# Optimization experiments

Hardware: AMD Instinct MI355X
Metric: run time of the kernel (lower is better)

## Reference

```python
import jax, jax.numpy as jnp
import numpy as np

N = 50000


def gcn_conv(x, edge_index, W, b):
    # x: [N, F_in], edge_index: [2, E] (row=source j, col=target i)
    n = x.shape[0]
    loops = jnp.arange(n, dtype=edge_index.dtype)
    row = jnp.concatenate([edge_index[0], loops])
    col = jnp.concatenate([edge_index[1], loops])
    # linear transform first (PyG GCNConv)
    xw = x @ W  # [N, F_out]
    # symmetric normalization deg^{-1/2}[row] * deg^{-1/2}[col]
    deg = jax.ops.segment_sum(jnp.ones_like(col, dtype=xw.dtype), col, num_segments=n)
    dis = jnp.where(deg > 0, jax.lax.rsqrt(jnp.maximum(deg, 1e-12)), 0.0)
    norm = dis[row] * dis[col]  # [E+N]
    # gather-scale-scatter: sum_j norm_ij * (W x_j)
    msgs = xw[row] * norm[:, None]
    out = jax.ops.segment_sum(msgs, col, num_segments=n)
    return out + b


def setup_inputs() -> dict:
    key = jax.random.key(0)
    k1, k2, k3, k4, k5 = jax.random.split(key, 5)
    in_dim, hidden_dim, out_dim = 128, 128, 64
    x = jax.random.normal(k1, (N, in_dim), dtype=jnp.float32)
    edge_index = jax.random.randint(k2, (2, 800000), 0, N, dtype=jnp.int64)
    s1 = 1.0 / np.sqrt(in_dim)
    s2 = 1.0 / np.sqrt(hidden_dim)
    W1 = jax.random.uniform(k3, (in_dim, hidden_dim), jnp.float32, -s1, s1)
    b1 = jnp.zeros((hidden_dim,), jnp.float32)
    W2 = jax.random.uniform(k4, (hidden_dim, out_dim), jnp.float32, -s2, s2)
    b2 = jnp.zeros((out_dim,), jnp.float32)
    return {"x": x, "edge_index": edge_index, "W1": W1, "b1": b1, "W2": W2, "b2": b2}


def reference(x, edge_index, W1, b1, W2, b2):
    h = gcn_conv(x, edge_index, W1, b1)
    h = jax.nn.relu(h)
    # dropout(p=0.5, training=False) -> identity (inference reference)
    out = gcn_conv(h, edge_index, W2, b2)
    return out
```

## Files before the change

kernel.cpp:

```cpp
#include <hip/hip_runtime.h>
#include <hip/hip_fp16.h>


typedef _Float16 half8 __attribute__((ext_vector_type(8)));
typedef float floatx4 __attribute__((ext_vector_type(4)));

__global__ void k_count(const int* __restrict__ col, int* __restrict__ deg,
                        int* __restrict__ rank, int E) {
    int e = blockIdx.x * blockDim.x + threadIdx.x;
    if (e < E) rank[e] = atomicAdd(&deg[col[e]], 1);
}

__global__ __launch_bounds__(1024) void k_scan_local(const int* __restrict__ deg,
                                                     int* __restrict__ rowptr,
                                                     int* __restrict__ bsum,
                                                     float* __restrict__ dis, int n) {
    __shared__ int s[1024];
    int b = blockIdx.x, tid = threadIdx.x;
    int i = b * 1024 + tid;
    int v = (i < n) ? deg[i] : 0;
    if (i < n) dis[i] = rsqrtf((float)v + 1.0f);
    s[tid] = v;
    __syncthreads();
    for (int off = 1; off < 1024; off <<= 1) {
        int t = (tid >= off) ? s[tid - off] : 0;
        __syncthreads();
        s[tid] += t;
        __syncthreads();
    }
    if (i < n) rowptr[i + 1] = s[tid];
    if (tid == 1023) bsum[b] = s[1023];
    if (b == 0 && tid == 0) rowptr[0] = 0;
}

__global__ __launch_bounds__(256) void k_scan_fix(int* __restrict__ rowptr,
                                                  const int* __restrict__ bsum, int n) {
    __shared__ int red[256];
    int b = blockIdx.x, tid = threadIdx.x;
    int partial = 0;
    for (int j = tid; j < b; j += 256) partial += bsum[j];
    red[tid] = partial;
    __syncthreads();
    for (int off = 128; off > 0; off >>= 1) {
        if (tid < off) red[tid] += red[tid + off];
        __syncthreads();
    }
    int offv = red[0];
    if (offv == 0) return;
#pragma unroll
    for (int r = 0; r < 4; ++r) {
        int i = b * 1024 + r * 256 + tid;
        if (i < n) rowptr[i + 1] += offv;
    }
}

__global__ void k_fill(const int* __restrict__ row, const int* __restrict__ col,
                       const int* __restrict__ rowptr, const int* __restrict__ rank,
                       int* __restrict__ csr, int E) {
    int e = blockIdx.x * blockDim.x + threadIdx.x;
    if (e < E) csr[rowptr[col[e]] + rank[e]] = row[e];
}

template <int N, typename AT>
__global__ __launch_bounds__(256) void k_gemm_mfma(const AT* __restrict__ X,
                                                   const float* __restrict__ W,
                                                   const float* __restrict__ scale,
                                                   __half* __restrict__ Y, int M) {
    __shared__ __align__(16) __half2 wt[N * 64];
    int tid = threadIdx.x;
    for (int i = tid; i < N * 64; i += 256) {
        int n = i & (N - 1);
        int k2 = i / N;
        float w0 = W[(size_t)(2 * k2) * N + n];
        float w1 = W[(size_t)(2 * k2 + 1) * N + n];
        wt[n * 64 + ((k2 >> 2) ^ (n & 15)) * 4 + (k2 & 3)] = __floats2half2_rn(w0, w1);
    }
    __syncthreads();

    int wid = tid >> 6, lane = tid & 63;
    int col = lane & 15, quad = lane >> 4;
    int m_a = blockIdx.x * 64 + wid * 16 + col;
    bool a_ok = m_a < M;
    constexpr int NT = N / 16;
    floatx4 acc[NT] = {};
#pragma unroll
    for (int ks = 0; ks < 4; ++ks) {
        int k = ks * 32 + quad * 8;
        half8 af;
        if constexpr (sizeof(AT) == 4) {
            floatx4 a0 = {0.f, 0.f, 0.f, 0.f}, a1 = {0.f, 0.f, 0.f, 0.f};
            if (a_ok) {
                a0 = *(const floatx4*)&X[(size_t)m_a * 128 + k];
                a1 = *(const floatx4*)&X[(size_t)m_a * 128 + k + 4];
            }
            af = half8{(_Float16)a0[0], (_Float16)a0[1], (_Float16)a0[2], (_Float16)a0[3],
                       (_Float16)a1[0], (_Float16)a1[1], (_Float16)a1[2], (_Float16)a1[3]};
        } else {
            half8 t = {};
            if (a_ok) t = *(const half8*)(const void*)&X[(size_t)m_a * 128 + k];
            af = t;
        }
        int kblk = ks * 4 + quad;
#pragma unroll
        for (int nt = 0; nt < NT; ++nt) {
            int n = nt * 16 + col;
            half8 bf = *(const half8*)(const void*)&wt[n * 64 + (kblk ^ (n & 15)) * 4];
            acc[nt] = __builtin_amdgcn_mfma_f32_16x16x32_f16(af, bf, acc[nt], 0, 0, 0);
        }
    }
    int mbase = blockIdx.x * 64 + wid * 16 + quad * 4;
    float s[4];
#pragma unroll
    for (int r = 0; r < 4; ++r) s[r] = (mbase + r < M) ? scale[mbase + r] : 0.f;
#pragma unroll
    for (int nt = 0; nt < NT; ++nt) {
#pragma unroll
        for (int r = 0; r < 4; ++r) {
            if (mbase + r < M)
                Y[(size_t)(mbase + r) * N + nt * 16 + col] = __float2half(acc[nt][r] * s[r]);
        }
    }
}

__global__ __launch_bounds__(256) void k_agg128(const __half* __restrict__ xw,
                                                const float* __restrict__ dis,
                                                const int* __restrict__ rowptr,
                                                const int* __restrict__ csr,
                                                const float* __restrict__ bias,
                                                __half* __restrict__ out, int n) {
    int tid = threadIdx.x;
    int lane = tid & 63;
    int q = lane >> 4, li = lane & 15;
    int node = blockIdx.x * 16 + ((tid >> 6) << 2) + q;
    bool ok = node < n;
    float di = 0.f;
    int beg = 0, end = 0;
    if (ok) {
        di = dis[node];
        beg = rowptr[node];
        end = rowptr[node + 1];
    }
    int deg = end - beg;
    int m1 = max(deg, __shfl(deg, lane ^ 16));
    int mx = max(m1, __shfl(m1, lane ^ 32));
    const half8* rows = (const half8*)xw;
    float acc[8] = {};
    if (ok) {
        half8 sf = rows[(size_t)node * 16 + li];
#pragma unroll
        for (int f = 0; f < 8; ++f) acc[f] = (float)sf[f];
    }
    int i = 0;
    for (; i + 8 <= mx; i += 8) {
        int s[8];
        half8 v[8];
#pragma unroll
        for (int j = 0; j < 8; ++j) {
            int e = beg + i + j;
            s[j] = (e < end) ? csr[e] : 0;
        }
#pragma unroll
        for (int j = 0; j < 8; ++j) v[j] = rows[(size_t)s[j] * 16 + li];
#pragma unroll
        for (int j = 0; j < 8; ++j) {
            if (beg + i + j < end) {
#pragma unroll
                for (int f = 0; f < 8; ++f) acc[f] += (float)v[j][f];
            }
        }
    }
    for (; i < mx; ++i) {
        int e = beg + i;
        int s = (e < end) ? csr[e] : 0;
        half8 v = rows[(size_t)s * 16 + li];
        if (e < end) {
#pragma unroll
            for (int f = 0; f < 8; ++f) acc[f] += (float)v[f];
        }
    }
    if (ok) {
        floatx4 b0 = *(const floatx4*)&bias[li * 8];
        floatx4 b1 = *(const floatx4*)&bias[li * 8 + 4];
        half8 o;
#pragma unroll
        for (int f = 0; f < 4; ++f) o[f] = (_Float16)fmaxf(acc[f] * di + b0[f], 0.f);
#pragma unroll
        for (int f = 0; f < 4; ++f) o[4 + f] = (_Float16)fmaxf(acc[4 + f] * di + b1[f], 0.f);
        ((half8*)out)[(size_t)node * 16 + li] = o;
    }
}

__global__ __launch_bounds__(256) void k_agg64(const __half* __restrict__ xw,
                                               const float* __restrict__ dis,
                                               const int* __restrict__ rowptr,
                                               const int* __restrict__ csr,
                                               const float* __restrict__ bias,
                                               float* __restrict__ out, int n) {
    int tid = threadIdx.x;
    int lane = tid & 63;
    int o8 = lane >> 3, li = lane & 7;
    int node = blockIdx.x * 32 + ((tid >> 6) << 3) + o8;
    bool ok = node < n;
    float di = 0.f;
    int beg = 0, end = 0;
    if (ok) {
        di = dis[node];
        beg = rowptr[node];
        end = rowptr[node + 1];
    }
    int deg = end - beg;
    int m1 = max(deg, __shfl(deg, lane ^ 8));
    int m2 = max(m1, __shfl(m1, lane ^ 16));
    int mx = max(m2, __shfl(m2, lane ^ 32));
    const half8* rows = (const half8*)xw;
    float acc[8] = {};
    if (ok) {
        half8 sf = rows[(size_t)node * 8 + li];
#pragma unroll
        for (int f = 0; f < 8; ++f) acc[f] = (float)sf[f];
    }
    int i = 0;
    for (; i + 8 <= mx; i += 8) {
        int s[8];
        half8 v[8];
#pragma unroll
        for (int j = 0; j < 8; ++j) {
            int e = beg + i + j;
            s[j] = (e < end) ? csr[e] : 0;
        }
#pragma unroll
        for (int j = 0; j < 8; ++j) v[j] = rows[(size_t)s[j] * 8 + li];
#pragma unroll
        for (int j = 0; j < 8; ++j) {
            if (beg + i + j < end) {
#pragma unroll
                for (int f = 0; f < 8; ++f) acc[f] += (float)v[j][f];
            }
        }
    }
    for (; i < mx; ++i) {
        int e = beg + i;
        int s = (e < end) ? csr[e] : 0;
        half8 v = rows[(size_t)s * 8 + li];
        if (e < end) {
#pragma unroll
            for (int f = 0; f < 8; ++f) acc[f] += (float)v[f];
        }
    }
    if (ok) {
        floatx4 b0 = *(const floatx4*)&bias[li * 8];
        floatx4 b1 = *(const floatx4*)&bias[li * 8 + 4];
        floatx4 o0, o1;
#pragma unroll
        for (int f = 0; f < 4; ++f) o0[f] = acc[f] * di + b0[f];
#pragma unroll
        for (int f = 0; f < 4; ++f) o1[f] = acc[4 + f] * di + b1[f];
        *(floatx4*)&out[(size_t)node * 64 + li * 8] = o0;
        *(floatx4*)&out[(size_t)node * 64 + li * 8 + 4] = o1;
    }
}

extern "C" void kernel_launch(void* const* d_in, const int* in_sizes, int n_in,
                              void* d_out, int out_size, void* d_ws, size_t ws_size,
                              hipStream_t stream) {
    const float* x  = (const float*)d_in[0];
    const int*   ei = (const int*)d_in[1];
    const float* W1 = (const float*)d_in[2];
    const float* b1 = (const float*)d_in[3];
    const float* W2 = (const float*)d_in[4];
    const float* b2 = (const float*)d_in[5];
    float* out = (float*)d_out;

    const int n = in_sizes[0] / 128;
    const int E = in_sizes[1] / 2;
    const int* row = ei;
    const int* col = ei + E;
    const int NB = (n + 1023) / 1024;

    char* ws = (char*)d_ws;
    size_t off = 0;
    auto alloc = [&](size_t bytes) -> void* {
        void* p = ws + off;
        off += (bytes + 255) & ~(size_t)255;
        return p;
    };
    int*    deg    = (int*)alloc((size_t)n * 4);
    int*    rowptr = (int*)alloc((size_t)(n + 1) * 4);
    int*    bsum   = (int*)alloc((size_t)NB * 4);
    int*    rank   = (int*)alloc((size_t)E * 4);
    int*    csr    = (int*)alloc((size_t)E * 4);
    float*  dis    = (float*)alloc((size_t)n * 4);
    __half* xw1    = (__half*)alloc((size_t)n * 128 * 2);
    __half* h      = (__half*)alloc((size_t)n * 128 * 2);
    __half* xw2    = (__half*)alloc((size_t)n * 64 * 2);
    (void)ws_size;

    hipMemsetAsync(deg, 0, (size_t)n * 4, stream);
    k_count<<<(E + 255) / 256, 256, 0, stream>>>(col, deg, rank, E);
    k_scan_local<<<NB, 1024, 0, stream>>>(deg, rowptr, bsum, dis, n);
    k_scan_fix<<<NB, 256, 0, stream>>>(rowptr, bsum, n);
    k_fill<<<(E + 255) / 256, 256, 0, stream>>>(row, col, rowptr, rank, csr, E);

    int gb = (n + 63) / 64;
    k_gemm_mfma<128, float><<<gb, 256, 0, stream>>>(x, W1, dis, xw1, n);
    k_agg128<<<(n + 15) / 16, 256, 0, stream>>>(xw1, dis, rowptr, csr, b1, h, n);

    k_gemm_mfma<64, __half><<<gb, 256, 0, stream>>>(h, W2, dis, xw2, n);
    k_agg64<<<(n + 31) / 32, 256, 0, stream>>>(xw2, dis, rowptr, csr, b2, out, n);
}
```

Baseline: 215.9 us.

## Fuse edge counting with first GEMM and store per-edge source norms in CSR

The degree-count atomics and the first MFMA GEMM now run as one launch, with blocks split by index, so the GEMM no longer depends on the degree scan. The GEMM drops its dis[row] scaling. Instead, the CSR fill stores each source's dis value next to its index as an int2, and the aggregation kernels apply that weight per edge; the bounds predicate is gone because padded entries carry a zero weight. This aims to overlap GEMM1 with the atomic counting pass and remove one kernel launch, at the cost of doubling CSR size and adding a multiply per feature per edge.

Result: slower. 226.5 us (+4.9%).

```diff
diff --git a/kernel.cpp b/kernel.cpp
--- a/kernel.cpp
+++ b/kernel.cpp
@@ -5,10 +5,80 @@
 typedef _Float16 half8 __attribute__((ext_vector_type(8)));
 typedef float floatx4 __attribute__((ext_vector_type(4)));
 
-__global__ void k_count(const int* __restrict__ col, int* __restrict__ deg,
-                        int* __restrict__ rank, int E) {
-    int e = blockIdx.x * blockDim.x + threadIdx.x;
-    if (e < E) rank[e] = atomicAdd(&deg[col[e]], 1);
+template <int N, typename AT>
+__device__ __forceinline__ void gemm_tile(const AT* __restrict__ X,
+                                          const float* __restrict__ W,
+                                          __half* __restrict__ Y, int M,
+                                          int m0, __half2* wt, int tid) {
+    for (int i = tid; i < N * 64; i += 256) {
+        int nn = i & (N - 1);
+        int k2 = i / N;
+        float w0 = W[(size_t)(2 * k2) * N + nn];
+        float w1 = W[(size_t)(2 * k2 + 1) * N + nn];
+        wt[nn * 64 + ((k2 >> 2) ^ (nn & 15)) * 4 + (k2 & 3)] = __floats2half2_rn(w0, w1);
+    }
+    __syncthreads();
+    int wid = tid >> 6, lane = tid & 63;
+    int col = lane & 15, quad = lane >> 4;
+    int m_a = m0 + wid * 16 + col;
+    bool a_ok = m_a < M;
+    constexpr int NT = N / 16;
+    floatx4 acc[NT] = {};
+#pragma unroll
+    for (int ks = 0; ks < 4; ++ks) {
+        int k = ks * 32 + quad * 8;
+        half8 af;
+        if constexpr (sizeof(AT) == 4) {
+            floatx4 a0 = {0.f, 0.f, 0.f, 0.f}, a1 = {0.f, 0.f, 0.f, 0.f};
+            if (a_ok) {
+                a0 = *(const floatx4*)&X[(size_t)m_a * 128 + k];
+                a1 = *(const floatx4*)&X[(size_t)m_a * 128 + k + 4];
+            }
+            af = half8{(_Float16)a0[0], (_Float16)a0[1], (_Float16)a0[2], (_Float16)a0[3],
+                       (_Float16)a1[0], (_Float16)a1[1], (_Float16)a1[2], (_Float16)a1[3]};
+        } else {
+            half8 t = {};
+            if (a_ok) t = *(const half8*)(const void*)&X[(size_t)m_a * 128 + k];
+            af = t;
+        }
+        int kblk = ks * 4 + quad;
+#pragma unroll
+        for (int nt = 0; nt < NT; ++nt) {
+            int nn = nt * 16 + col;
+            half8 bf = *(const half8*)(const void*)&wt[nn * 64 + (kblk ^ (nn & 15)) * 4];
+            acc[nt] = __builtin_amdgcn_mfma_f32_16x16x32_f16(af, bf, acc[nt], 0, 0, 0);
+        }
+    }
+    int mbase = m0 + wid * 16 + quad * 4;
+#pragma unroll
+    for (int nt = 0; nt < NT; ++nt) {
+#pragma unroll
+        for (int r = 0; r < 4; ++r) {
+            if (mbase + r < M)
+                Y[(size_t)(mbase + r) * N + nt * 16 + col] = __float2half(acc[nt][r]);
+        }
+    }
+}
+
+__global__ __launch_bounds__(256) void k_count_gemm1(
+    const int* __restrict__ col, int* __restrict__ deg, int* __restrict__ rank, int E,
+    const float* __restrict__ X, const float* __restrict__ W1,
+    __half* __restrict__ Y, int M, int CB) {
+    __shared__ __align__(16) __half2 wt[128 * 64];
+    int b = blockIdx.x, tid = threadIdx.x;
+    if (b < CB) {
+        int e = b * 256 + tid;
+        if (e < E) rank[e] = atomicAdd(&deg[col[e]], 1);
+        return;
+    }
+    gemm_tile<128, float>(X, W1, Y, M, (b - CB) * 64, wt, tid);
+}
+
+__global__ __launch_bounds__(256) void k_gemm2(const __half* __restrict__ X,
+                                               const float* __restrict__ W,
+                                               __half* __restrict__ Y, int M) {
+    __shared__ __align__(16) __half2 wt[64 * 64];
+    gemm_tile<64, __half>(X, W, Y, M, blockIdx.x * 64, wt, threadIdx.x);
 }
 
 __global__ __launch_bounds__(1024) void k_scan_local(const int* __restrict__ deg,
@@ -56,76 +126,18 @@
 
 __global__ void k_fill(const int* __restrict__ row, const int* __restrict__ col,
                        const int* __restrict__ rowptr, const int* __restrict__ rank,
-                       int* __restrict__ csr, int E) {
+                       const float* __restrict__ dis, int2* __restrict__ csrw, int E) {
     int e = blockIdx.x * blockDim.x + threadIdx.x;
-    if (e < E) csr[rowptr[col[e]] + rank[e]] = row[e];
-}
-
-template <int N, typename AT>
-__global__ __launch_bounds__(256) void k_gemm_mfma(const AT* __restrict__ X,
-                                                   const float* __restrict__ W,
-                                                   const float* __restrict__ scale,
-                                                   __half* __restrict__ Y, int M) {
-    __shared__ __align__(16) __half2 wt[N * 64];
-    int tid = threadIdx.x;
-    for (int i = tid; i < N * 64; i += 256) {
-        int n = i & (N - 1);
-        int k2 = i / N;
-        float w0 = W[(size_t)(2 * k2) * N + n];
-        float w1 = W[(size_t)(2 * k2 + 1) * N + n];
-        wt[n * 64 + ((k2 >> 2) ^ (n & 15)) * 4 + (k2 & 3)] = __floats2half2_rn(w0, w1);
-    }
-    __syncthreads();
-
-    int wid = tid >> 6, lane = tid & 63;
-    int col = lane & 15, quad = lane >> 4;
-    int m_a = blockIdx.x * 64 + wid * 16 + col;
-    bool a_ok = m_a < M;
-    constexpr int NT = N / 16;
-    floatx4 acc[NT] = {};
-#pragma unroll
-    for (int ks = 0; ks < 4; ++ks) {
-        int k = ks * 32 + quad * 8;
-        half8 af;
-        if constexpr (sizeof(AT) == 4) {
-            floatx4 a0 = {0.f, 0.f, 0.f, 0.f}, a1 = {0.f, 0.f, 0.f, 0.f};
-            if (a_ok) {
-                a0 = *(const floatx4*)&X[(size_t)m_a * 128 + k];
-                a1 = *(const floatx4*)&X[(size_t)m_a * 128 + k + 4];
-            }
-            af = half8{(_Float16)a0[0], (_Float16)a0[1], (_Float16)a0[2], (_Float16)a0[3],
-                       (_Float16)a1[0], (_Float16)a1[1], (_Float16)a1[2], (_Float16)a1[3]};
-        } else {
-            half8 t = {};
-            if (a_ok) t = *(const half8*)(const void*)&X[(size_t)m_a * 128 + k];
-            af = t;
-        }
-        int kblk = ks * 4 + quad;
-#pragma unroll
-        for (int nt = 0; nt < NT; ++nt) {
-            int n = nt * 16 + col;
-            half8 bf = *(const half8*)(const void*)&wt[n * 64 + (kblk ^ (n & 15)) * 4];
-            acc[nt] = __builtin_amdgcn_mfma_f32_16x16x32_f16(af, bf, acc[nt], 0, 0, 0);
-        }
-    }
-    int mbase = blockIdx.x * 64 + wid * 16 + quad * 4;
-    float s[4];
-#pragma unroll
-    for (int r = 0; r < 4; ++r) s[r] = (mbase + r < M) ? scale[mbase + r] : 0.f;
-#pragma unroll
-    for (int nt = 0; nt < NT; ++nt) {
-#pragma unroll
-        for (int r = 0; r < 4; ++r) {
-            if (mbase + r < M)
-                Y[(size_t)(mbase + r) * N + nt * 16 + col] = __float2half(acc[nt][r] * s[r]);
-        }
+    if (e < E) {
+        int r = row[e];
+        csrw[rowptr[col[e]] + rank[e]] = make_int2(r, __float_as_int(dis[r]));
     }
 }
 
 __global__ __launch_bounds__(256) void k_agg128(const __half* __restrict__ xw,
                                                 const float* __restrict__ dis,
                                                 const int* __restrict__ rowptr,
-                                                const int* __restrict__ csr,
+                                                const int2* __restrict__ csrw,
                                                 const float* __restrict__ bias,
                                                 __half* __restrict__ out, int n) {
     int tid = threadIdx.x;
@@ -140,43 +152,43 @@
         beg = rowptr[node];
         end = rowptr[node + 1];
     }
-    int deg = end - beg;
-    int m1 = max(deg, __shfl(deg, lane ^ 16));
+    int dg = end - beg;
+    int m1 = max(dg, __shfl(dg, lane ^ 16));
     int mx = max(m1, __shfl(m1, lane ^ 32));
     const half8* rows = (const half8*)xw;
     float acc[8] = {};
     if (ok) {
         half8 sf = rows[(size_t)node * 16 + li];
 #pragma unroll
-        for (int f = 0; f < 8; ++f) acc[f] = (float)sf[f];
+        for (int f = 0; f < 8; ++f) acc[f] = di * (float)sf[f];
     }
     int i = 0;
     for (; i + 8 <= mx; i += 8) {
         int s[8];
+        float w[8];
         half8 v[8];
 #pragma unroll
         for (int j = 0; j < 8; ++j) {
             int e = beg + i + j;
-            s[j] = (e < end) ? csr[e] : 0;
+            int2 cw = (e < end) ? csrw[e] : make_int2(0, 0);
+            s[j] = cw.x;
+            w[j] = __int_as_float(cw.y);
         }
 #pragma unroll
         for (int j = 0; j < 8; ++j) v[j] = rows[(size_t)s[j] * 16 + li];
 #pragma unroll
         for (int j = 0; j < 8; ++j) {
-            if (beg + i + j < end) {
-#pragma unroll
-                for (int f = 0; f < 8; ++f) acc[f] += (float)v[j][f];
-            }
+#pragma unroll
+            for (int f = 0; f < 8; ++f) acc[f] += w[j] * (float)v[j][f];
         }
     }
     for (; i < mx; ++i) {
         int e = beg + i;
-        int s = (e < end) ? csr[e] : 0;
-        half8 v = rows[(size_t)s * 16 + li];
-        if (e < end) {
-#pragma unroll
-            for (int f = 0; f < 8; ++f) acc[f] += (float)v[f];
-        }
+        int2 cw = (e < end) ? csrw[e] : make_int2(0, 0);
+        half8 v = rows[(size_t)cw.x * 16 + li];
+        float w = __int_as_float(cw.y);
+#pragma unroll
+        for (int f = 0; f < 8; ++f) acc[f] += w * (float)v[f];
     }
     if (ok) {
         floatx4 b0 = *(const floatx4*)&bias[li * 8];
@@ -193,7 +205,7 @@
 __global__ __launch_bounds__(256) void k_agg64(const __half* __restrict__ xw,
                                                const float* __restrict__ dis,
                                                const int* __restrict__ rowptr,
-                                               const int* __restrict__ csr,
+                                               const int2* __restrict__ csrw,
                                                const float* __restrict__ bias,
                                                float* __restrict__ out, int n) {
     int tid = threadIdx.x;
@@ -208,8 +220,8 @@
         beg = rowptr[node];
         end = rowptr[node + 1];
     }
-    int deg = end - beg;
-    int m1 = max(deg, __shfl(deg, lane ^ 8));
+    int dg = end - beg;
+    int m1 = max(dg, __shfl(dg, lane ^ 8));
     int m2 = max(m1, __shfl(m1, lane ^ 16));
     int mx = max(m2, __shfl(m2, lane ^ 32));
     const half8* rows = (const half8*)xw;
@@ -217,35 +229,35 @@
     if (ok) {
         half8 sf = rows[(size_t)node * 8 + li];
 #pragma unroll
-        for (int f = 0; f < 8; ++f) acc[f] = (float)sf[f];
+        for (int f = 0; f < 8; ++f) acc[f] = di * (float)sf[f];
     }
     int i = 0;
     for (; i + 8 <= mx; i += 8) {
         int s[8];
+        float w[8];
         half8 v[8];
 #pragma unroll
         for (int j = 0; j < 8; ++j) {
             int e = beg + i + j;
-            s[j] = (e < end) ? csr[e] : 0;
+            int2 cw = (e < end) ? csrw[e] : make_int2(0, 0);
+            s[j] = cw.x;
+            w[j] = __int_as_float(cw.y);
         }
 #pragma unroll
         for (int j = 0; j < 8; ++j) v[j] = rows[(size_t)s[j] * 8 + li];
 #pragma unroll
         for (int j = 0; j < 8; ++j) {
-            if (beg + i + j < end) {
-#pragma unroll
-                for (int f = 0; f < 8; ++f) acc[f] += (float)v[j][f];
-            }
+#pragma unroll
+            for (int f = 0; f < 8; ++f) acc[f] += w[j] * (float)v[j][f];
         }
     }
     for (; i < mx; ++i) {
         int e = beg + i;
-        int s = (e < end) ? csr[e] : 0;
-        half8 v = rows[(size_t)s * 8 + li];
-        if (e < end) {
-#pragma unroll
-            for (int f = 0; f < 8; ++f) acc[f] += (float)v[f];
-        }
+        int2 cw = (e < end) ? csrw[e] : make_int2(0, 0);
+        half8 v = rows[(size_t)cw.x * 8 + li];
+        float w = __int_as_float(cw.y);
+#pragma unroll
+        for (int f = 0; f < 8; ++f) acc[f] += w * (float)v[f];
     }
     if (ok) {
         floatx4 b0 = *(const floatx4*)&bias[li * 8];
@@ -276,6 +288,8 @@
     const int* row = ei;
     const int* col = ei + E;
     const int NB = (n + 1023) / 1024;
+    const int CB = (E + 255) / 256;
+    const int GB = (n + 63) / 64;
 
     char* ws = (char*)d_ws;
     size_t off = 0;
@@ -288,7 +302,7 @@
     int*    rowptr = (int*)alloc((size_t)(n + 1) * 4);
     int*    bsum   = (int*)alloc((size_t)NB * 4);
     int*    rank   = (int*)alloc((size_t)E * 4);
-    int*    csr    = (int*)alloc((size_t)E * 4);
+    int2*   csrw   = (int2*)alloc((size_t)E * 8);
     float*  dis    = (float*)alloc((size_t)n * 4);
     __half* xw1    = (__half*)alloc((size_t)n * 128 * 2);
     __half* h      = (__half*)alloc((size_t)n * 128 * 2);
@@ -296,15 +310,12 @@
     (void)ws_size;
 
     hipMemsetAsync(deg, 0, (size_t)n * 4, stream);
-    k_count<<<(E + 255) / 256, 256, 0, stream>>>(col, deg, rank, E);
+    k_count_gemm1<<<CB + GB, 256, 0, stream>>>(col, deg, rank, E, x, W1, xw1, n, CB);
     k_scan_local<<<NB, 1024, 0, stream>>>(deg, rowptr, bsum, dis, n);
     k_scan_fix<<<NB, 256, 0, stream>>>(rowptr, bsum, n);
-    k_fill<<<(E + 255) / 256, 256, 0, stream>>>(row, col, rowptr, rank, csr, E);
-
-    int gb = (n + 63) / 64;
-    k_gemm_mfma<128, float><<<gb, 256, 0, stream>>>(x, W1, dis, xw1, n);
-    k_agg128<<<(n + 15) / 16, 256, 0, stream>>>(xw1, dis, rowptr, csr, b1, h, n);
-
-    k_gemm_mfma<64, __half><<<gb, 256, 0, stream>>>(h, W2, dis, xw2, n);
-    k_agg64<<<(n + 31) / 32, 256, 0, stream>>>(xw2, dis, rowptr, csr, b2, out, n);
-}
+    k_fill<<<CB, 256, 0, stream>>>(row, col, rowptr, rank, dis, csrw, E);
+
+    k_agg128<<<(n + 15) / 16, 256, 0, stream>>>(xw1, dis, rowptr, csrw, b1, h, n);
+    k_gemm2<<<GB, 256, 0, stream>>>(h, W2, xw2, n);
+    k_agg64<<<(n + 31) / 32, 256, 0, stream>>>(xw2, dis, rowptr, csrw, b2, out, n);
+}
```

## Use single-block scan and cooperative shuffle-based neighbor index loads in aggregation

Applied to the files above, without the earlier changes.

Replaces the two-kernel multi-block prefix scan (local scan plus fix-up) with one 1024-thread block that scans per-thread chunks, removing a launch and the bsum buffer. In both aggregation kernels, each lane now loads one CSR neighbor index and the indices are broadcast with shuffles, replacing redundant per-lane loads of all eight indices. The scalar tail loop is merged into the main 8-wide loop. The single-block scan serializes about 49 elements per thread with strided non-coalesced reads, which may cost more than the removed launch.

New measurement: 327.2 us. 1.52x slower.

```diff
diff --git a/kernel.cpp b/kernel.cpp
--- a/kernel.cpp
+++ b/kernel.cpp
@@ -11,46 +11,36 @@
     if (e < E) rank[e] = atomicAdd(&deg[col[e]], 1);
 }
 
-__global__ __launch_bounds__(1024) void k_scan_local(const int* __restrict__ deg,
-                                                     int* __restrict__ rowptr,
-                                                     int* __restrict__ bsum,
-                                                     float* __restrict__ dis, int n) {
-    __shared__ int s[1024];
-    int b = blockIdx.x, tid = threadIdx.x;
-    int i = b * 1024 + tid;
-    int v = (i < n) ? deg[i] : 0;
-    if (i < n) dis[i] = rsqrtf((float)v + 1.0f);
-    s[tid] = v;
+__global__ __launch_bounds__(1024) void k_scan1(const int* __restrict__ deg,
+                                                int* __restrict__ rowptr,
+                                                float* __restrict__ dis, int n) {
+    __shared__ int part[1024];
+    int t = threadIdx.x;
+    const int PER = (n + 1023) >> 10;
+    int base = t * PER;
+    int sum = 0;
+    for (int j = 0; j < PER; ++j) {
+        int idx = base + j;
+        int v = (idx < n) ? deg[idx] : 0;
+        if (idx < n) dis[idx] = rsqrtf((float)v + 1.0f);
+        sum += v;
+    }
+    part[t] = sum;
     __syncthreads();
     for (int off = 1; off < 1024; off <<= 1) {
-        int t = (tid >= off) ? s[tid - off] : 0;
+        int v = (t >= off) ? part[t - off] : 0;
         __syncthreads();
-        s[tid] += t;
+        part[t] += v;
         __syncthreads();
     }
-    if (i < n) rowptr[i + 1] = s[tid];
-    if (tid == 1023) bsum[b] = s[1023];
-    if (b == 0 && tid == 0) rowptr[0] = 0;
-}
-
-__global__ __launch_bounds__(256) void k_scan_fix(int* __restrict__ rowptr,
-                                                  const int* __restrict__ bsum, int n) {
-    __shared__ int red[256];
-    int b = blockIdx.x, tid = threadIdx.x;
-    int partial = 0;
-    for (int j = tid; j < b; j += 256) partial += bsum[j];
-    red[tid] = partial;
-    __syncthreads();
-    for (int off = 128; off > 0; off >>= 1) {
-        if (tid < off) red[tid] += red[tid + off];
-        __syncthreads();
-    }
-    int offv = red[0];
-    if (offv == 0) return;
-#pragma unroll
-    for (int r = 0; r < 4; ++r) {
-        int i = b * 1024 + r * 256 + tid;
-        if (i < n) rowptr[i + 1] += offv;
+    int run = (t > 0) ? part[t - 1] : 0;
+    if (t == 0) rowptr[0] = 0;
+    for (int j = 0; j < PER; ++j) {
+        int idx = base + j;
+        if (idx < n) {
+            run += deg[idx];
+            rowptr[idx + 1] = run;
+        }
     }
 }
 
@@ -69,14 +59,13 @@
     __shared__ __align__(16) __half2 wt[N * 64];
     int tid = threadIdx.x;
     for (int i = tid; i < N * 64; i += 256) {
-        int n = i & (N - 1);
+        int nn = i & (N - 1);
         int k2 = i / N;
-        float w0 = W[(size_t)(2 * k2) * N + n];
-        float w1 = W[(size_t)(2 * k2 + 1) * N + n];
-        wt[n * 64 + ((k2 >> 2) ^ (n & 15)) * 4 + (k2 & 3)] = __floats2half2_rn(w0, w1);
+        float w0 = W[(size_t)(2 * k2) * N + nn];
+        float w1 = W[(size_t)(2 * k2 + 1) * N + nn];
+        wt[nn * 64 + ((k2 >> 2) ^ (nn & 15)) * 4 + (k2 & 3)] = __floats2half2_rn(w0, w1);
     }
     __syncthreads();
-
     int wid = tid >> 6, lane = tid & 63;
     int col = lane & 15, quad = lane >> 4;
     int m_a = blockIdx.x * 64 + wid * 16 + col;
@@ -103,8 +92,8 @@
         int kblk = ks * 4 + quad;
 #pragma unroll
         for (int nt = 0; nt < NT; ++nt) {
-            int n = nt * 16 + col;
-            half8 bf = *(const half8*)(const void*)&wt[n * 64 + (kblk ^ (n & 15)) * 4];
+            int nn = nt * 16 + col;
+            half8 bf = *(const half8*)(const void*)&wt[nn * 64 + (kblk ^ (nn & 15)) * 4];
             acc[nt] = __builtin_amdgcn_mfma_f32_16x16x32_f16(af, bf, acc[nt], 0, 0, 0);
         }
     }
@@ -131,6 +120,7 @@
     int tid = threadIdx.x;
     int lane = tid & 63;
     int q = lane >> 4, li = lane & 15;
+    int qbase = lane & 48;
     int node = blockIdx.x * 16 + ((tid >> 6) << 2) + q;
     bool ok = node < n;
     float di = 0.f;
@@ -140,8 +130,8 @@
         beg = rowptr[node];
         end = rowptr[node + 1];
     }
-    int deg = end - beg;
-    int m1 = max(deg, __shfl(deg, lane ^ 16));
+    int dg = end - beg;
+    int m1 = max(dg, __shfl(dg, lane ^ 16));
     int mx = max(m1, __shfl(m1, lane ^ 32));
     const half8* rows = (const half8*)xw;
     float acc[8] = {};
@@ -150,32 +140,21 @@
 #pragma unroll
         for (int f = 0; f < 8; ++f) acc[f] = (float)sf[f];
     }
-    int i = 0;
-    for (; i + 8 <= mx; i += 8) {
-        int s[8];
+    for (int i = 0; i < mx; i += 8) {
+        int e = beg + i + (li & 7);
+        int myidx = (e < end) ? csr[e] : 0;
         half8 v[8];
 #pragma unroll
         for (int j = 0; j < 8; ++j) {
-            int e = beg + i + j;
-            s[j] = (e < end) ? csr[e] : 0;
-        }
-#pragma unroll
-        for (int j = 0; j < 8; ++j) v[j] = rows[(size_t)s[j] * 16 + li];
+            int s = __shfl(myidx, qbase + j);
+            v[j] = rows[(size_t)s * 16 + li];
+        }
 #pragma unroll
         for (int j = 0; j < 8; ++j) {
             if (beg + i + j < end) {
 #pragma unroll
                 for (int f = 0; f < 8; ++f) acc[f] += (float)v[j][f];
             }
-        }
-    }
-    for (; i < mx; ++i) {
-        int e = beg + i;
-        int s = (e < end) ? csr[e] : 0;
-        half8 v = rows[(size_t)s * 16 + li];
-        if (e < end) {
-#pragma unroll
-            for (int f = 0; f < 8; ++f) acc[f] += (float)v[f];
         }
     }
     if (ok) {
@@ -199,6 +178,7 @@
     int tid = threadIdx.x;
     int lane = tid & 63;
     int o8 = lane >> 3, li = lane & 7;
+    int obase = lane & 56;
     int node = blockIdx.x * 32 + ((tid >> 6) << 3) + o8;
     bool ok = node < n;
     float di = 0.f;
@@ -208,8 +188,8 @@
         beg = rowptr[node];
         end = rowptr[node + 1];
     }
-    int deg = end - beg;
-    int m1 = max(deg, __shfl(deg, lane ^ 8));
+    int dg = end - beg;
+    int m1 = max(dg, __shfl(dg, lane ^ 8));
     int m2 = max(m1, __shfl(m1, lane ^ 16));
     int mx = max(m2, __shfl(m2, lane ^ 32));
     const half8* rows = (const half8*)xw;
@@ -219,17 +199,15 @@
 #pragma unroll
         for (int f = 0; f < 8; ++f) acc[f] = (float)sf[f];
     }
-    int i = 0;
-    for (; i + 8 <= mx; i += 8) {
-        int s[8];
+    for (int i = 0; i < mx; i += 8) {
+        int e = beg + i + li;
+        int myidx = (e < end) ? csr[e] : 0;
         half8 v[8];
 #pragma unroll
         for (int j = 0; j < 8; ++j) {
-            int e = beg + i + j;
-            s[j] = (e < end) ? csr[e] : 0;
-        }
-#pragma unroll
-        for (int j = 0; j < 8; ++j) v[j] = rows[(size_t)s[j] * 8 + li];
+            int s = __shfl(myidx, obase + j);
+            v[j] = rows[(size_t)s * 8 + li];
+        }
 #pragma unroll
         for (int j = 0; j < 8; ++j) {
             if (beg + i + j < end) {
@@ -238,25 +216,16 @@
             }
         }
     }
-    for (; i < mx; ++i) {
-        int e = beg + i;
-        int s = (e < end) ? csr[e] : 0;
-        half8 v = rows[(size_t)s * 8 + li];
-        if (e < end) {
-#pragma unroll
-            for (int f = 0; f < 8; ++f) acc[f] += (float)v[f];
-        }
-    }
     if (ok) {
         floatx4 b0 = *(const floatx4*)&bias[li * 8];
         floatx4 b1 = *(const floatx4*)&bias[li * 8 + 4];
-        floatx4 o0, o1;
-#pragma unroll
-        for (int f = 0; f < 4; ++f) o0[f] = acc[f] * di + b0[f];
-#pragma unroll
-        for (int f = 0; f < 4; ++f) o1[f] = acc[4 + f] * di + b1[f];
-        *(floatx4*)&out[(size_t)node * 64 + li * 8] = o0;
-        *(floatx4*)&out[(size_t)node * 64 + li * 8 + 4] = o1;
+        floatx4 out0, out1;
+#pragma unroll
+        for (int f = 0; f < 4; ++f) out0[f] = acc[f] * di + b0[f];
+#pragma unroll
+        for (int f = 0; f < 4; ++f) out1[f] = acc[4 + f] * di + b1[f];
+        *(floatx4*)&out[(size_t)node * 64 + li * 8] = out0;
+        *(floatx4*)&out[(size_t)node * 64 + li * 8 + 4] = out1;
     }
 }
 
@@ -275,7 +244,8 @@
     const int E = in_sizes[1] / 2;
     const int* row = ei;
     const int* col = ei + E;
-    const int NB = (n + 1023) / 1024;
+    const int CB = (E + 255) / 256;
+    const int GB = (n + 63) / 64;
 
     char* ws = (char*)d_ws;
     size_t off = 0;
@@ -286,7 +256,6 @@
     };
     int*    deg    = (int*)alloc((size_t)n * 4);
     int*    rowptr = (int*)alloc((size_t)(n + 1) * 4);
-    int*    bsum   = (int*)alloc((size_t)NB * 4);
     int*    rank   = (int*)alloc((size_t)E * 4);
     int*    csr    = (int*)alloc((size_t)E * 4);
     float*  dis    = (float*)alloc((size_t)n * 4);
@@ -296,15 +265,12 @@
     (void)ws_size;
 
     hipMemsetAsync(deg, 0, (size_t)n * 4, stream);
-    k_count<<<(E + 255) / 256, 256, 0, stream>>>(col, deg, rank, E);
-    k_scan_local<<<NB, 1024, 0, stream>>>(deg, rowptr, bsum, dis, n);
-    k_scan_fix<<<NB, 256, 0, stream>>>(rowptr, bsum, n);
-    k_fill<<<(E + 255) / 256, 256, 0, stream>>>(row, col, rowptr, rank, csr, E);
-
-    int gb = (n + 63) / 64;
-    k_gemm_mfma<128, float><<<gb, 256, 0, stream>>>(x, W1, dis, xw1, n);
+    k_count<<<CB, 256, 0, stream>>>(col, deg, rank, E);
+    k_scan1<<<1, 1024, 0, stream>>>(deg, rowptr, dis, n);
+    k_fill<<<CB, 256, 0, stream>>>(row, col, rowptr, rank, csr, E);
+
+    k_gemm_mfma<128, float><<<GB, 256, 0, stream>>>(x, W1, dis, xw1, n);
     k_agg128<<<(n + 15) / 16, 256, 0, stream>>>(xw1, dis, rowptr, csr, b1, h, n);
-
-    k_gemm_mfma<64, __half><<<gb, 256, 0, stream>>>(h, W2, dis, xw2, n);
+    k_gemm_mfma<64, __half><<<GB, 256, 0, stream>>>(h, W2, dis, xw2, n);
     k_agg64<<<(n + 31) / 32, 256, 0, stream>>>(xw2, dis, rowptr, csr, b2, out, n);
 }
```
